# Kernel optimization log

Hardware: AMD Instinct MI355X
Metric: run time of the kernel (lower is better)

Reference implementation:

```python
import jax, jax.numpy as jnp
import numpy as np
from jax import lax


def _lstm(x, h, c, W, U, b):
    # torch LSTM gate order: i, f, g, o; b = b_ih + b_hh combined
    g = x @ W.T + h @ U.T + b
    i, f, gg, o = jnp.split(g, 4, axis=-1)
    c2 = jax.nn.sigmoid(f) * c + jax.nn.sigmoid(i) * jnp.tanh(gg)
    h2 = jax.nn.sigmoid(o) * jnp.tanh(c2)
    return h2, c2


def _run_dir(x, mask, W, U, b):
    # packed-sequence semantics: state updates only where mask, outputs 0 at pad
    B = x.shape[0]
    Hh = U.shape[1]
    h0 = jnp.zeros((B, Hh), x.dtype)

    def step(carry, inp):
        h, c = carry
        xt, mt = inp
        h2, c2 = _lstm(xt, h, c, W, U, b)
        m = mt[:, None]
        h = jnp.where(m, h2, h)
        c = jnp.where(m, c2, c)
        return (h, c), jnp.where(m, h, jnp.zeros_like(h))

    (hf, cf), outs = lax.scan(step, (h0, h0), (jnp.swapaxes(x, 0, 1), mask.T))
    return jnp.swapaxes(outs, 0, 1), hf, cf  # (B,S,H), (B,H), (B,H)


def _forward(source, source_mask, target, target_mask, emb_src, emb_tgt,
             eW0f, eU0f, eb0f, eW0b, eU0b, eb0b,
             eW1f, eU1f, eb1f, eW1b, eU1b, eb1b,
             dW0, dU0, db0, dW1, dU1, db1, wW, wb):
    x = emb_src[source]  # (B,S,D)
    finals_h, finals_c = [], []
    enc_params = [(eW0f, eU0f, eb0f, eW0b, eU0b, eb0b),
                  (eW1f, eU1f, eb1f, eW1b, eU1b, eb1b)]
    for Wf, Uf, bf, Wb, Ub, bb in enc_params:
        of, hf, cf = _run_dir(x, source_mask, Wf, Uf, bf)
        # backward direction: reverse time; prefix mask becomes suffix, so the
        # masked-update scan exactly reproduces packed reverse-direction LSTM
        ob, hb, cb = _run_dir(x[:, ::-1], source_mask[:, ::-1], Wb, Ub, bb)
        ob = ob[:, ::-1]
        x = jnp.concatenate([of, ob], axis=-1)
        finals_h.append(jnp.concatenate([hf, hb], axis=-1))  # (B, 2H)
        finals_c.append(jnp.concatenate([cf, cb], axis=-1))

    # decoder initial state: per-layer concat of fwd/bwd encoder final states
    xt = emb_tgt[target]  # (B,T,D)

    def dstep(carry, inp):
        h1, c1, h2, c2 = carry
        t, mt = inp
        m = mt[:, None]
        nh1, nc1 = _lstm(t, h1, c1, dW0, dU0, db0)
        h1 = jnp.where(m, nh1, h1)
        c1 = jnp.where(m, nc1, c1)
        nh2, nc2 = _lstm(h1, h2, c2, dW1, dU1, db1)
        h2 = jnp.where(m, nh2, h2)
        c2 = jnp.where(m, nc2, c2)
        return (h1, c1, h2, c2), jnp.where(m, h2, jnp.zeros_like(h2))

    init = (finals_h[0], finals_c[0], finals_h[1], finals_c[1])
    _, outs = lax.scan(dstep, init, (jnp.swapaxes(xt, 0, 1), target_mask.T))
    outs = jnp.swapaxes(outs, 0, 1)  # (B,T,d_out)
    return jnp.einsum('btd,vd->btv', outs, wW) + wb  # (B,T,V)


def setup_inputs() -> dict:
    key = jax.random.key(0)
    ks = jax.random.split(key, 32)
    B, S, T, V, D, H = 32, 64, 65, 32000, 256, 512
    DO = 2 * H

    def p(i, shape):
        return jax.random.normal(ks[i], shape, dtype=jnp.float32) * 0.05

    source = jax.random.randint(ks[0], (B, S), 0, V + 1)
    target = jax.random.randint(ks[1], (B, T), 0, V + 1)
    # descending-sorted lengths -> sort/perm in the original is identity
    slen = jnp.sort(jax.random.randint(ks[2], (B,), 1, S + 1))[::-1]
    tlen = jnp.sort(jax.random.randint(ks[3], (B,), 1, T + 1))[::-1]
    source_mask = jnp.arange(S)[None, :] < slen[:, None]
    target_mask = jnp.arange(T)[None, :] < tlen[:, None]
    emb = p(4, (V + 1, D))
    return dict(
        source=source, source_mask=source_mask, target=target, target_mask=target_mask,
        emb_src=emb, emb_tgt=emb + 0.0,
        eW0f=p(5, (4 * H, D)), eU0f=p(6, (4 * H, H)), eb0f=p(7, (4 * H,)),
        eW0b=p(8, (4 * H, D)), eU0b=p(9, (4 * H, H)), eb0b=p(10, (4 * H,)),
        eW1f=p(11, (4 * H, 2 * H)), eU1f=p(12, (4 * H, H)), eb1f=p(13, (4 * H,)),
        eW1b=p(14, (4 * H, 2 * H)), eU1b=p(15, (4 * H, H)), eb1b=p(16, (4 * H,)),
        dW0=p(17, (4 * DO, D)), dU0=p(18, (4 * DO, DO)), db0=p(19, (4 * DO,)),
        dW1=p(20, (4 * DO, DO)), dU1=p(21, (4 * DO, DO)), db1=p(22, (4 * DO,)),
        wW=p(23, (V, DO)), wb=p(24, (V,)))


def reference(source, source_mask, target, target_mask, emb_src, emb_tgt,
              eW0f, eU0f, eb0f, eW0b, eU0b, eb0b,
              eW1f, eU1f, eb1f, eW1b, eU1b, eb1b,
              dW0, dU0, db0, dW1, dU1, db1, wW, wb):
    return _forward(source, source_mask, target, target_mask, emb_src, emb_tgt,
                    eW0f, eU0f, eb0f, eW0b, eU0b, eb0b,
                    eW1f, eU1f, eb1f, eW1b, eU1b, eb1b,
                    dW0, dU0, db0, dW1, dU1, db1, wW, wb)
```

## Files before the change

kernel.cpp:

```cpp
#include <hip/hip_runtime.h>

#define B_ 32
#define S_ 64
#define T_ 65
#define D_ 256
#define HE 512
#define HD 1024
#define VV 32000

typedef __attribute__((ext_vector_type(8))) short bf16x8;
typedef __attribute__((ext_vector_type(4))) float f32x4;

__device__ inline unsigned short f2bf(float f) {
  unsigned int u = __float_as_uint(f);
  u += 0x7FFFu + ((u >> 16) & 1u);
  return (unsigned short)(u >> 16);
}
__device__ inline float sigmf(float x) { return 1.0f / (1.0f + __expf(-x)); }

#define MFMA16(a,b,c) __builtin_amdgcn_mfma_f32_16x16x32_bf16((a),(b),(c),0,0,0)

#define SLOT_STRIDE 32
__device__ inline void sigwait(int* slots, int* rel, int nblk, int e, int bid) {
  asm volatile("s_waitcnt vmcnt(0)" ::: "memory");
  __syncthreads();
  const int tid = threadIdx.x;
  if (bid == 0) {
    if (tid < nblk) {
      if (tid == 0)
        __hip_atomic_store(&slots[0], e, __ATOMIC_RELAXED,
                           __HIP_MEMORY_SCOPE_AGENT);
      while (__hip_atomic_load(&slots[tid * SLOT_STRIDE], __ATOMIC_RELAXED,
                               __HIP_MEMORY_SCOPE_AGENT) < e)
        __builtin_amdgcn_s_sleep(2);
    }
    __syncthreads();
    if (tid == 0)
      __hip_atomic_store(rel, e, __ATOMIC_RELAXED, __HIP_MEMORY_SCOPE_AGENT);
  } else {
    if (tid == 0) {
      __hip_atomic_store(&slots[bid * SLOT_STRIDE], e, __ATOMIC_RELAXED,
                         __HIP_MEMORY_SCOPE_AGENT);
      while (__hip_atomic_load(rel, __ATOMIC_RELAXED,
                               __HIP_MEMORY_SCOPE_AGENT) < e)
        __builtin_amdgcn_s_sleep(2);
    }
    __syncthreads();
  }
}

__device__ inline int swz(int row, int col, int LD) {
  return row * LD + ((((col >> 3) ^ (row & 7)) << 3) | (col & 7));
}
template <int LD, int NU64>
__device__ inline void stage_h(short* h_lds, const short* src) {
  unsigned long long* s = (unsigned long long*)src;
  const int tid = threadIdx.x;
#pragma unroll
  for (int base = 0; base < NU64 / 256; base += 16) {
    unsigned long long tmp[16];
#pragma unroll
    for (int i = 0; i < 16; i++) {
      if (base + i < NU64 / 256)
        tmp[i] = __hip_atomic_load(&s[(base + i) * 256 + tid], __ATOMIC_RELAXED,
                                   __HIP_MEMORY_SCOPE_AGENT);
    }
#pragma unroll
    for (int i = 0; i < 16; i++) {
      if (base + i < NU64 / 256) {
        int o = ((base + i) * 256 + tid) * 4;
        *(unsigned long long*)(h_lds + swz(o / LD, o % LD, LD)) = tmp[i];
      }
    }
  }
}

__device__ inline int mask_dtype(const unsigned char* m) {
  unsigned b0 = m[0], b1 = m[1], b2 = m[2], b3 = m[3], b4 = m[4];
  if (b0 == 1 && b1 == 1) return 0;
  if (b0 == 1) {
    if (b4 == 1) return 1;
    if (b4 == 0 && m[8] == 1) return 2;
    return 1;
  }
  if (b0 == 0x80 && b1 == 0x3F) return 4;
  if (b0 == 0x00 && b1 == 0x3C) return 5;
  if (b2 == 0x80 && b3 == 0x3F) return 3;
  return 1;
}
__device__ inline int mask_val(const unsigned char* m, int dt, int i) {
  switch (dt) {
    case 0: return m[i] != 0;
    case 1: return ((const int*)m)[i] != 0;
    case 2: return ((const long long*)m)[i] != 0;
    case 3: return ((const float*)m)[i] != 0.0f;
    default: return ((const unsigned short*)m)[i] != 0;
  }
}
__global__ void k_masks(const unsigned char* msrc, const unsigned char* mtgt,
                        signed char* o_src, signed char* o_tgt) {
  const unsigned char* m = blockIdx.x ? mtgt : msrc;
  signed char* o = blockIdx.x ? o_tgt : o_src;
  int n = blockIdx.x ? (B_ * T_) : (B_ * S_);
  int dt = mask_dtype(m);
  for (int i = threadIdx.x; i < n; i += blockDim.x)
    o[i] = (signed char)mask_val(m, dt, i);
}

struct CvtJobs {
  const float* src[13];
  short* dst[13];
  int n4[13];
};
__global__ __launch_bounds__(256) void k_convert(CvtJobs jb) {
  int j = blockIdx.y;
  const float4* s = (const float4*)jb.src[j];
  ushort4* d = (ushort4*)jb.dst[j];
  int n4 = jb.n4[j];
  for (int i = blockIdx.x * blockDim.x + threadIdx.x; i < n4;
       i += gridDim.x * blockDim.x) {
    float4 v = s[i];
    ushort4 o;
    o.x = f2bf(v.x); o.y = f2bf(v.y); o.z = f2bf(v.z); o.w = f2bf(v.w);
    d[i] = o;
  }
}

__global__ __launch_bounds__(256) void k_gather(const int* sids, const int* tids,
                                                const float* es, const float* et,
                                                short* Xs, short* Xt) {
  int job = blockIdx.y;
  int rows = job ? (B_ * T_) : (B_ * S_);
  const int* ids = job ? tids : sids;
  const float* emb = job ? et : es;
  ushort4* X = (ushort4*)(job ? Xt : Xs);
  int total = rows * (D_ / 4);
  for (int i = blockIdx.x * blockDim.x + threadIdx.x; i < total;
       i += gridDim.x * blockDim.x) {
    int row = i >> 6;
    int c4 = i & 63;
    long id = ids[row];
    float4 v = ((const float4*)(emb + id * (long)D_))[c4];
    ushort4 o;
    o.x = f2bf(v.x); o.y = f2bf(v.y); o.z = f2bf(v.z); o.w = f2bf(v.w);
    X[(long)row * 64 + c4] = o;
  }
}

template <bool B_F32, bool C_F32>
__global__ __launch_bounds__(256) void k_gemm(const short* __restrict__ A,
                                              const short* __restrict__ Bw,
                                              const float* __restrict__ Bwf,
                                              const float* __restrict__ bias,
                                              short* __restrict__ C,
                                              float* __restrict__ Cf,
                                              int M_out, int N, int K) {
  __shared__ short As[128 * 32];
  __shared__ short Bs[128 * 32];
  const int tid = threadIdx.x;
  const int wave = tid >> 6, lane = tid & 63;
  const int wm = wave >> 1, wn = wave & 1;
  const int r16 = lane & 15, kb = lane >> 4;
  const long m0 = (long)blockIdx.y * 128;
  const long n0 = (long)blockIdx.x * 128;

  const int ch0 = tid * 2, ch1 = ch0 + 1;
  const int ar0 = ch0 >> 2, ak0 = (ch0 & 3) * 8;
  const int ar1 = ch1 >> 2, ak1 = (ch1 & 3) * 8;

  f32x4 acc[4][4];
#pragma unroll
  for (int i = 0; i < 4; i++)
#pragma unroll
    for (int j = 0; j < 4; j++) acc[i][j] = (f32x4){0.f, 0.f, 0.f, 0.f};

  for (int kt = 0; kt < K; kt += 32) {
    bf16x8 va0 = *(const bf16x8*)(A + (m0 + ar0) * K + kt + ak0);
    bf16x8 va1 = *(const bf16x8*)(A + (m0 + ar1) * K + kt + ak1);
    bf16x8 vb0, vb1;
    if (B_F32) {
      const float* p0 = Bwf + (n0 + ar0) * K + kt + ak0;
      const float* p1 = Bwf + (n0 + ar1) * K + kt + ak1;
      float4 x0 = *(const float4*)p0, x1 = *(const float4*)(p0 + 4);
      float4 y0 = *(const float4*)p1, y1 = *(const float4*)(p1 + 4);
      vb0 = (bf16x8){(short)f2bf(x0.x), (short)f2bf(x0.y), (short)f2bf(x0.z),
                     (short)f2bf(x0.w), (short)f2bf(x1.x), (short)f2bf(x1.y),
                     (short)f2bf(x1.z), (short)f2bf(x1.w)};
      vb1 = (bf16x8){(short)f2bf(y0.x), (short)f2bf(y0.y), (short)f2bf(y0.z),
                     (short)f2bf(y0.w), (short)f2bf(y1.x), (short)f2bf(y1.y),
                     (short)f2bf(y1.z), (short)f2bf(y1.w)};
    } else {
      vb0 = *(const bf16x8*)(Bw + (n0 + ar0) * K + kt + ak0);
      vb1 = *(const bf16x8*)(Bw + (n0 + ar1) * K + kt + ak1);
    }
    __syncthreads();
    *(bf16x8*)(As + ar0 * 32 + ak0) = va0;
    *(bf16x8*)(As + ar1 * 32 + ak1) = va1;
    *(bf16x8*)(Bs + ar0 * 32 + ak0) = vb0;
    *(bf16x8*)(Bs + ar1 * 32 + ak1) = vb1;
    __syncthreads();
    bf16x8 av[4], bv[4];
#pragma unroll
    for (int i = 0; i < 4; i++)
      av[i] = *(const bf16x8*)(As + (wm * 64 + i * 16 + r16) * 32 + kb * 8);
#pragma unroll
    for (int j = 0; j < 4; j++)
      bv[j] = *(const bf16x8*)(Bs + (wn * 64 + j * 16 + r16) * 32 + kb * 8);
#pragma unroll
    for (int i = 0; i < 4; i++)
#pragma unroll
      for (int j = 0; j < 4; j++) acc[i][j] = MFMA16(av[i], bv[j], acc[i][j]);
  }
#pragma unroll
  for (int j = 0; j < 4; j++) {
    long gc = n0 + wn * 64 + j * 16 + r16;
    float bb = bias ? bias[gc] : 0.f;
#pragma unroll
    for (int i = 0; i < 4; i++) {
      long gr0 = m0 + wm * 64 + i * 16 + kb * 4;
#pragma unroll
      for (int r = 0; r < 4; r++) {
        long gr = gr0 + r;
        if (gr < M_out) {
          if (C_F32) Cf[gr * N + gc] = acc[i][j][r] + bb;
          else C[gr * N + gc] = (short)f2bf(acc[i][j][r] + bb);
        }
      }
    }
  }
}

__global__ __launch_bounds__(256) void k_enc_persist(
    const short* __restrict__ Wf, const short* __restrict__ Wb_,
    short* __restrict__ H, const float* __restrict__ Pf,
    const float* __restrict__ Pb, short* __restrict__ Outb, int outLD,
    int outOffDir, float* __restrict__ Cfin,
    const signed char* __restrict__ msk, int* slots, int* rel) {
  const int dir = blockIdx.y;
  const short* W = dir ? Wb_ : Wf;
  const float* P = dir ? Pb : Pf;
  int* slotsD = slots + dir * 32 * SLOT_STRIDE;
  int* relD = rel + dir * SLOT_STRIDE;
  const int q = threadIdx.x >> 6, lane = threadIdx.x & 63;
  const int r16 = lane & 15, kb = lane >> 4;
  const int n = q * HE + blockIdx.x * 16 + r16;
  const short* wr = W + (size_t)n * HE;
  const int bb = threadIdx.x >> 3;
  const int cp = threadIdx.x & 7;
  const int j0 = blockIdx.x * 16 + 2 * cp;
  __shared__ short h_lds[32 * HE];
  __shared__ float g_lds[4][2][16][16];
  float creg0 = 0.f, creg1 = 0.f;

  for (int s = 0; s < S_; ++s) {
    const int t = dir ? (S_ - 1 - s) : s;
    const int rp = s & 1;
    const short* Ar = H + ((size_t)rp * 2 + dir) * (B_ * HE);
    short* Hw = H + ((size_t)(rp ^ 1) * 2 + dir) * (B_ * HE);

    __syncthreads();
    stage_h<HE, 4096>(h_lds, Ar);
    __syncthreads();

    f32x4 acc0 = (f32x4){0.f, 0.f, 0.f, 0.f};
    f32x4 acc1 = (f32x4){0.f, 0.f, 0.f, 0.f};
#pragma unroll 8
    for (int k = kb * 8; k < HE; k += 32) {
      bf16x8 bv = *(const bf16x8*)(wr + k);
      bf16x8 a0 = *(const bf16x8*)(h_lds + swz(r16, k, HE));
      bf16x8 a1 = *(const bf16x8*)(h_lds + swz(16 + r16, k, HE));
      acc0 = MFMA16(a0, bv, acc0);
      acc1 = MFMA16(a1, bv, acc1);
    }
#pragma unroll
    for (int r = 0; r < 4; r++) {
      g_lds[q][0][kb * 4 + r][r16] = acc0[r];
      g_lds[q][1][kb * 4 + r][r16] = acc1[r];
    }
    __syncthreads();
    {
      const int mt = bb >> 4, br = bb & 15;
      const float* pr = P + (size_t)(bb * S_ + t) * (4 * HE);
      bool valid = msk[bb * S_ + t] != 0;
      unsigned int hv;
      float h2v[2];
#pragma unroll
      for (int cc = 0; cc < 2; ++cc) {
        int j = j0 + cc;
        float g0 = g_lds[0][mt][br][2 * cp + cc] + pr[j];
        float g1 = g_lds[1][mt][br][2 * cp + cc] + pr[HE + j];
        float g2 = g_lds[2][mt][br][2 * cp + cc] + pr[2 * HE + j];
        float g3 = g_lds[3][mt][br][2 * cp + cc] + pr[3 * HE + j];
        float co = cc ? creg1 : creg0;
        float c2 = sigmf(g1) * co + sigmf(g0) * tanhf(g2);
        float h2 = sigmf(g3) * tanhf(c2);
        if (valid) { if (cc) creg1 = c2; else creg0 = c2; }
        h2v[cc] = h2;
      }
      unsigned short o0 = valid ? f2bf(h2v[0])
                                : (unsigned short)h_lds[swz(bb, j0, HE)];
      unsigned short o1 = valid ? f2bf(h2v[1])
                                : (unsigned short)h_lds[swz(bb, j0 + 1, HE)];
      hv = (unsigned int)o0 | ((unsigned int)o1 << 16);
      __hip_atomic_store((unsigned int*)(Hw + bb * HE + j0), hv,
                         __ATOMIC_RELAXED, __HIP_MEMORY_SCOPE_AGENT);
      if (Outb) {
        unsigned int ov = valid ? hv : 0u;
        *(unsigned int*)(Outb + (size_t)(bb * S_ + t) * outLD +
                         outOffDir * dir + j0) = ov;
      }
    }
    if (s < S_ - 1) sigwait(slotsD, relD, 32, s + 1, blockIdx.x);
  }
  Cfin[(size_t)(dir * B_ + bb) * HE + j0] = creg0;
  Cfin[(size_t)(dir * B_ + bb) * HE + j0 + 1] = creg1;
}

__global__ __launch_bounds__(256) void k_dec_persist(
    const short* __restrict__ dU0b, const short* __restrict__ dW1b,
    const short* __restrict__ dU1b, short* __restrict__ H1,
    short* __restrict__ H2, const float* __restrict__ Q0,
    const float* __restrict__ db1f, const float* __restrict__ dC1i,
    const float* __restrict__ dC2i, short* __restrict__ douts,
    const signed char* __restrict__ msk, int* slots, int* rel) {
  const int role = blockIdx.y;
  const int bid = role * 64 + blockIdx.x;
  const int q = threadIdx.x >> 6, lane = threadIdx.x & 63;
  const int r16 = lane & 15, kb = lane >> 4;
  const int n = q * HD + blockIdx.x * 16 + r16;
  const int bb = threadIdx.x >> 3;
  const int cp = threadIdx.x & 7;
  const int j0 = blockIdx.x * 16 + 2 * cp;
  __shared__ short h_lds[32 * HD];
  __shared__ float g_lds[4][2][16][16];
  const float* Ci = role ? dC2i : dC1i;
  float creg0 = Ci[(size_t)bb * HD + j0];
  float creg1 = Ci[(size_t)bb * HD + j0 + 1];
  const short* w0 = dU0b + (size_t)n * HD;
  const short* w1 = dW1b + (size_t)n * HD;
  const short* w2 = dU1b + (size_t)n * HD;

  for (int k = 0; k <= T_; ++k) {
    if (role == 0 && k <= T_ - 1) {
      const int t = k, rp = k & 1;
      const short* Ar = H1 + (size_t)rp * (B_ * HD);
      short* Hw = H1 + (size_t)(rp ^ 1) * (B_ * HD);
      __syncthreads();
      stage_h<HD, 8192>(h_lds, Ar);
      __syncthreads();
      f32x4 acc0 = (f32x4){0.f, 0.f, 0.f, 0.f};
      f32x4 acc1 = (f32x4){0.f, 0.f, 0.f, 0.f};
#pragma unroll 8
      for (int kk = kb * 8; kk < HD; kk += 32) {
        bf16x8 bv = *(const bf16x8*)(w0 + kk);
        bf16x8 a0 = *(const bf16x8*)(h_lds + swz(r16, kk, HD));
        bf16x8 a1 = *(const bf16x8*)(h_lds + swz(16 + r16, kk, HD));
        acc0 = MFMA16(a0, bv, acc0);
        acc1 = MFMA16(a1, bv, acc1);
      }
#pragma unroll
      for (int r = 0; r < 4; r++) {
        g_lds[q][0][kb * 4 + r][r16] = acc0[r];
        g_lds[q][1][kb * 4 + r][r16] = acc1[r];
      }
      __syncthreads();
      {
        const int mt = bb >> 4, br = bb & 15;
        const float* pr = Q0 + (size_t)(bb * T_ + t) * (4 * HD);
        bool valid = msk[bb * T_ + t] != 0;
        float h2v[2];
#pragma unroll
        for (int cc = 0; cc < 2; ++cc) {
          int j = j0 + cc;
          float g0 = g_lds[0][mt][br][2 * cp + cc] + pr[j];
          float g1 = g_lds[1][mt][br][2 * cp + cc] + pr[HD + j];
          float g2 = g_lds[2][mt][br][2 * cp + cc] + pr[2 * HD + j];
          float g3 = g_lds[3][mt][br][2 * cp + cc] + pr[3 * HD + j];
          float co = cc ? creg1 : creg0;
          float c2 = sigmf(g1) * co + sigmf(g0) * tanhf(g2);
          float h2 = sigmf(g3) * tanhf(c2);
          if (valid) { if (cc) creg1 = c2; else creg0 = c2; }
          h2v[cc] = h2;
        }
        unsigned short o0 = valid ? f2bf(h2v[0])
                                  : (unsigned short)h_lds[swz(bb, j0, HD)];
        unsigned short o1 = valid ? f2bf(h2v[1])
                                  : (unsigned short)h_lds[swz(bb, j0 + 1, HD)];
        unsigned int hv = (unsigned int)o0 | ((unsigned int)o1 << 16);
        __hip_atomic_store((unsigned int*)(Hw + bb * HD + j0), hv,
                           __ATOMIC_RELAXED, __HIP_MEMORY_SCOPE_AGENT);
      }
    } else if (role == 1 && k >= 1) {
      const int t = k - 1, rp = t & 1;
      const short* X = H1 + (size_t)(k & 1) * (B_ * HD);
      const short* Ar2 = H2 + (size_t)rp * (B_ * HD);
      short* Hw = H2 + (size_t)(rp ^ 1) * (B_ * HD);
      f32x4 acc0 = (f32x4){0.f, 0.f, 0.f, 0.f};
      f32x4 acc1 = (f32x4){0.f, 0.f, 0.f, 0.f};
      __syncthreads();
      stage_h<HD, 8192>(h_lds, X);
      __syncthreads();
#pragma unroll 8
      for (int kk = kb * 8; kk < HD; kk += 32) {
        bf16x8 bv = *(const bf16x8*)(w1 + kk);
        bf16x8 a0 = *(const bf16x8*)(h_lds + swz(r16, kk, HD));
        bf16x8 a1 = *(const bf16x8*)(h_lds + swz(16 + r16, kk, HD));
        acc0 = MFMA16(a0, bv, acc0);
        acc1 = MFMA16(a1, bv, acc1);
      }
      __syncthreads();
      stage_h<HD, 8192>(h_lds, Ar2);
      __syncthreads();
#pragma unroll 8
      for (int kk = kb * 8; kk < HD; kk += 32) {
        bf16x8 bv = *(const bf16x8*)(w2 + kk);
        bf16x8 a0 = *(const bf16x8*)(h_lds + swz(r16, kk, HD));
        bf16x8 a1 = *(const bf16x8*)(h_lds + swz(16 + r16, kk, HD));
        acc0 = MFMA16(a0, bv, acc0);
        acc1 = MFMA16(a1, bv, acc1);
      }
#pragma unroll
      for (int r = 0; r < 4; r++) {
        g_lds[q][0][kb * 4 + r][r16] = acc0[r];
        g_lds[q][1][kb * 4 + r][r16] = acc1[r];
      }
      __syncthreads();
      {
        const int mt = bb >> 4, br = bb & 15;
        bool valid = msk[bb * T_ + t] != 0;
        float h2v[2];
#pragma unroll
        for (int cc = 0; cc < 2; ++cc) {
          int j = j0 + cc;
          float g0 = g_lds[0][mt][br][2 * cp + cc] + db1f[j];
          float g1 = g_lds[1][mt][br][2 * cp + cc] + db1f[HD + j];
          float g2 = g_lds[2][mt][br][2 * cp + cc] + db1f[2 * HD + j];
          float g3 = g_lds[3][mt][br][2 * cp + cc] + db1f[3 * HD + j];
          float co = cc ? creg1 : creg0;
          float c2 = sigmf(g1) * co + sigmf(g0) * tanhf(g2);
          float h2 = sigmf(g3) * tanhf(c2);
          if (valid) { if (cc) creg1 = c2; else creg0 = c2; }
          h2v[cc] = h2;
        }
        unsigned short o0 = valid ? f2bf(h2v[0])
                                  : (unsigned short)h_lds[swz(bb, j0, HD)];
        unsigned short o1 = valid ? f2bf(h2v[1])
                                  : (unsigned short)h_lds[swz(bb, j0 + 1, HD)];
        unsigned int hv = (unsigned int)o0 | ((unsigned int)o1 << 16);
        __hip_atomic_store((unsigned int*)(Hw + bb * HD + j0), hv,
                           __ATOMIC_RELAXED, __HIP_MEMORY_SCOPE_AGENT);
        *(unsigned int*)(douts + (size_t)(bb * T_ + t) * HD + j0) =
            valid ? hv : 0u;
      }
    }
    if (k < T_) sigwait(slots, rel, 128, k + 1, bid);
  }
}

__global__ __launch_bounds__(256) void k_decinit(const short* h0, const float* c0,
                                                 const short* h1, const float* c1f,
                                                 short* dh1, float* dc1,
                                                 short* dh2, float* dc2) {
  int i = blockIdx.x * 256 + threadIdx.x;
  if (i < B_ * HD) {
    int b = i >> 10, nn = i & 1023, d = nn >> 9, jj = nn & 511;
    int src = (d * B_ + b) * HE + jj;
    dh1[i] = h0[src];
    dc1[i] = c0[src];
    dh2[i] = h1[src];
    dc2[i] = c1f[src];
  }
}

extern "C" void kernel_launch(void* const* d_in, const int* in_sizes, int n_in,
                              void* d_out, int out_size, void* d_ws, size_t ws_size,
                              hipStream_t stream) {
  const int* src = (const int*)d_in[0];
  const unsigned char* msrc = (const unsigned char*)d_in[1];
  const int* tgt = (const int*)d_in[2];
  const unsigned char* mtgt = (const unsigned char*)d_in[3];
  const float* emb_s = (const float*)d_in[4];
  const float* emb_t = (const float*)d_in[5];
  const float* eW0f = (const float*)d_in[6];
  const float* eU0f = (const float*)d_in[7];
  const float* eb0f = (const float*)d_in[8];
  const float* eW0b = (const float*)d_in[9];
  const float* eU0b = (const float*)d_in[10];
  const float* eb0b = (const float*)d_in[11];
  const float* eW1f = (const float*)d_in[12];
  const float* eU1f = (const float*)d_in[13];
  const float* eb1f = (const float*)d_in[14];
  const float* eW1b = (const float*)d_in[15];
  const float* eU1b = (const float*)d_in[16];
  const float* eb1b = (const float*)d_in[17];
  const float* dW0 = (const float*)d_in[18];
  const float* dU0 = (const float*)d_in[19];
  const float* db0 = (const float*)d_in[20];
  const float* dW1 = (const float*)d_in[21];
  const float* dU1 = (const float*)d_in[22];
  const float* db1 = (const float*)d_in[23];
  const float* wW = (const float*)d_in[24];
  const float* wb = (const float*)d_in[25];
  (void)n_in; (void)in_sizes; (void)out_size; (void)ws_size;

  short* douts = (short*)d_ws;
  short* wW_b = (short*)((char*)d_ws + (size_t)2176 * 1024 * 2);

  char* po = (char*)d_out;
  size_t off = 0;
  auto alloc = [&](size_t bytes) -> char* {
    char* p = po + off;
    off += (bytes + 255) & ~(size_t)255;
    return p;
  };
  const size_t szW[12] = {
      (size_t)2048 * 256 * 2,  (size_t)2048 * 512 * 2,
      (size_t)2048 * 256 * 2,  (size_t)2048 * 512 * 2,
      (size_t)2048 * 1024 * 2, (size_t)2048 * 512 * 2,
      (size_t)2048 * 1024 * 2, (size_t)2048 * 512 * 2,
      (size_t)4096 * 256 * 2,  (size_t)4096 * 1024 * 2,
      (size_t)4096 * 1024 * 2, (size_t)4096 * 1024 * 2};
  short* Wb[12];
  for (int i = 0; i < 12; i++) Wb[i] = (short*)alloc(szW[i]);
  short* eW0f_b = Wb[0], *eU0f_b = Wb[1], *eW0b_b = Wb[2], *eU0b_b = Wb[3];
  short* eW1f_b = Wb[4], *eU1f_b = Wb[5], *eW1b_b = Wb[6], *eU1b_b = Wb[7];
  short* dW0_b = Wb[8], *dU0_b = Wb[9], *dW1_b = Wb[10], *dU1_b = Wb[11];
  short* Xs_b = (short*)alloc((size_t)2048 * 256 * 2);
  short* Xt_b = (short*)alloc((size_t)2176 * 256 * 2);
  short* X1_b = (short*)alloc((size_t)2048 * 1024 * 2);
  char* uni = alloc((size_t)2176 * 4096 * 4);
  float* P0f = (float*)uni;
  float* P0b = P0f + (size_t)2048 * 2048;
  float* P1f = (float*)uni;
  float* P1b = P1f + (size_t)2048 * 2048;
  float* Q0 = (float*)uni;
  char* zero_begin = po + off;
  int* slots_e0 = (int*)alloc(2 * 32 * SLOT_STRIDE * 4);
  int* rel_e0 = (int*)alloc(2 * SLOT_STRIDE * 4);
  int* slots_e1 = (int*)alloc(2 * 32 * SLOT_STRIDE * 4);
  int* rel_e1 = (int*)alloc(2 * SLOT_STRIDE * 4);
  int* slots_d = (int*)alloc(128 * SLOT_STRIDE * 4);
  int* rel_d = (int*)alloc(SLOT_STRIDE * 4);
  short* encH0 = (short*)alloc((size_t)2 * 2 * B_ * HE * 2);
  short* encH1 = (short*)alloc((size_t)2 * 2 * B_ * HE * 2);
  size_t zero_bytes = (size_t)((po + off) - zero_begin);
  float* Cfin0 = (float*)alloc((size_t)2 * B_ * HE * 4);
  float* Cfin1 = (float*)alloc((size_t)2 * B_ * HE * 4);
  short* dH1 = (short*)alloc((size_t)2 * B_ * HD * 2);
  short* dH2 = (short*)alloc((size_t)2 * B_ * HD * 2);
  float* dC1f = (float*)alloc((size_t)B_ * HD * 4);
  float* dC2f = (float*)alloc((size_t)B_ * HD * 4);
  signed char* msk_s = (signed char*)alloc(B_ * S_);
  signed char* msk_t = (signed char*)alloc(B_ * T_);

  const float* FN = nullptr;

  (void)hipMemsetAsync(douts, 0, (size_t)2176 * 1024 * 2, stream);
  (void)hipMemsetAsync(zero_begin, 0, zero_bytes, stream);
  k_masks<<<dim3(2), dim3(256), 0, stream>>>(msrc, mtgt, msk_s, msk_t);
  CvtJobs jb;
  const float* srcs[13] = {eW0f, eU0f, eW0b, eU0b, eW1f, eU1f,
                           eW1b, eU1b, dW0, dU0, dW1, dU1, wW};
  short* dsts[13] = {Wb[0], Wb[1], Wb[2], Wb[3], Wb[4], Wb[5],
                     Wb[6], Wb[7], Wb[8], Wb[9], Wb[10], Wb[11], wW_b};
  int ns[13] = {2048 * 256, 2048 * 512, 2048 * 256, 2048 * 512,
                2048 * 1024, 2048 * 512, 2048 * 1024, 2048 * 512,
                4096 * 256, 4096 * 1024, 4096 * 1024, 4096 * 1024, VV * 1024};
  for (int i = 0; i < 13; i++) { jb.src[i] = srcs[i]; jb.dst[i] = dsts[i]; jb.n4[i] = ns[i] / 4; }
  k_convert<<<dim3(1024, 13), 256, 0, stream>>>(jb);
  k_gather<<<dim3(544, 2), 256, 0, stream>>>(src, tgt, emb_s, emb_t, Xs_b, Xt_b);

  k_gemm<false, true><<<dim3(16, 16), 256, 0, stream>>>(
      Xs_b, eW0f_b, FN, eb0f, (short*)nullptr, P0f, 2048, 2048, 256);
  k_gemm<false, true><<<dim3(16, 16), 256, 0, stream>>>(
      Xs_b, eW0b_b, FN, eb0b, (short*)nullptr, P0b, 2048, 2048, 256);

  k_enc_persist<<<dim3(32, 2), 256, 0, stream>>>(
      eU0f_b, eU0b_b, encH0, P0f, P0b, X1_b, 1024, 512, Cfin0, msk_s,
      slots_e0, rel_e0);

  k_gemm<false, true><<<dim3(16, 16), 256, 0, stream>>>(
      X1_b, eW1f_b, FN, eb1f, (short*)nullptr, P1f, 2048, 2048, 1024);
  k_gemm<false, true><<<dim3(16, 16), 256, 0, stream>>>(
      X1_b, eW1b_b, FN, eb1b, (short*)nullptr, P1b, 2048, 2048, 1024);

  k_enc_persist<<<dim3(32, 2), 256, 0, stream>>>(
      eU1f_b, eU1b_b, encH1, P1f, P1b, (short*)nullptr, 0, 0, Cfin1, msk_s,
      slots_e1, rel_e1);

  k_decinit<<<dim3(128), 256, 0, stream>>>(encH0, Cfin0, encH1, Cfin1,
                                           dH1, dC1f, dH2, dC2f);

  k_gemm<false, true><<<dim3(32, 17), 256, 0, stream>>>(
      Xt_b, dW0_b, FN, db0, (short*)nullptr, Q0, 2176, 4096, 256);

  k_dec_persist<<<dim3(64, 2), 256, 0, stream>>>(
      dU0_b, dW1_b, dU1_b, dH1, dH2, Q0, db1, dC1f, dC2f, douts, msk_t,
      slots_d, rel_d);

  k_gemm<false, true><<<dim3(250, 17), 256, 0, stream>>>(
      douts, wW_b, FN, wb, (short*)nullptr, (float*)d_out, B_ * T_, VV, 1024);
}
```

Measured before the change: 2.175 ms.

## Use all-to-all flag barrier and stage both decoder layer-2 inputs at once

Replaces the master-block gather/release grid barrier with a flat barrier in which every block publishes its step counter and polls all peers' slots directly. This removes one serialized round trip through block 0 per recurrent step. In the decoder layer-2 role, the input h1 and recurrent h2 are staged into two separate LDS buffers in one pass, and a single interleaved MFMA loop replaces the two sequential staging and compute phases. This removes a barrier and staging round, but doubles decoder LDS use to about 128KB per block and adds polling traffic from every block.

```diff
diff --git a/kernel.cpp b/kernel.cpp
--- a/kernel.cpp
+++ b/kernel.cpp
@@ -21,56 +21,68 @@
 #define MFMA16(a,b,c) __builtin_amdgcn_mfma_f32_16x16x32_bf16((a),(b),(c),0,0,0)
 
 #define SLOT_STRIDE 32
-__device__ inline void sigwait(int* slots, int* rel, int nblk, int e, int bid) {
+__device__ inline void gbar_all(int* slots, int nblk, int e, int bid) {
   asm volatile("s_waitcnt vmcnt(0)" ::: "memory");
   __syncthreads();
   const int tid = threadIdx.x;
-  if (bid == 0) {
-    if (tid < nblk) {
-      if (tid == 0)
-        __hip_atomic_store(&slots[0], e, __ATOMIC_RELAXED,
-                           __HIP_MEMORY_SCOPE_AGENT);
-      while (__hip_atomic_load(&slots[tid * SLOT_STRIDE], __ATOMIC_RELAXED,
-                               __HIP_MEMORY_SCOPE_AGENT) < e)
-        __builtin_amdgcn_s_sleep(2);
-    }
-    __syncthreads();
-    if (tid == 0)
-      __hip_atomic_store(rel, e, __ATOMIC_RELAXED, __HIP_MEMORY_SCOPE_AGENT);
-  } else {
-    if (tid == 0) {
-      __hip_atomic_store(&slots[bid * SLOT_STRIDE], e, __ATOMIC_RELAXED,
-                         __HIP_MEMORY_SCOPE_AGENT);
-      while (__hip_atomic_load(rel, __ATOMIC_RELAXED,
-                               __HIP_MEMORY_SCOPE_AGENT) < e)
-        __builtin_amdgcn_s_sleep(2);
-    }
-    __syncthreads();
-  }
+  if (tid == 0)
+    __hip_atomic_store(&slots[bid * SLOT_STRIDE], e, __ATOMIC_RELAXED,
+                       __HIP_MEMORY_SCOPE_AGENT);
+  if (tid < nblk) {
+    while (__hip_atomic_load(&slots[tid * SLOT_STRIDE], __ATOMIC_RELAXED,
+                             __HIP_MEMORY_SCOPE_AGENT) < e)
+      __builtin_amdgcn_s_sleep(2);
+  }
+  __syncthreads();
 }
 
 __device__ inline int swz(int row, int col, int LD) {
   return row * LD + ((((col >> 3) ^ (row & 7)) << 3) | (col & 7));
 }
 template <int LD, int NU64>
-__device__ inline void stage_h(short* h_lds, const short* src) {
-  unsigned long long* s = (unsigned long long*)src;
+__device__ inline void stage1(short* lds, const short* src) {
+  const unsigned long long* s = (const unsigned long long*)src;
   const int tid = threadIdx.x;
-#pragma unroll
-  for (int base = 0; base < NU64 / 256; base += 16) {
-    unsigned long long tmp[16];
-#pragma unroll
-    for (int i = 0; i < 16; i++) {
-      if (base + i < NU64 / 256)
-        tmp[i] = __hip_atomic_load(&s[(base + i) * 256 + tid], __ATOMIC_RELAXED,
-                                   __HIP_MEMORY_SCOPE_AGENT);
-    }
-#pragma unroll
-    for (int i = 0; i < 16; i++) {
-      if (base + i < NU64 / 256) {
-        int o = ((base + i) * 256 + tid) * 4;
-        *(unsigned long long*)(h_lds + swz(o / LD, o % LD, LD)) = tmp[i];
-      }
+  constexpr int NPT = NU64 / 256;
+  unsigned long long tmp[NPT];
+#pragma unroll
+  for (int i = 0; i < NPT; i++)
+    tmp[i] = __hip_atomic_load(&s[i * 256 + tid], __ATOMIC_RELAXED,
+                               __HIP_MEMORY_SCOPE_AGENT);
+#pragma unroll
+  for (int i = 0; i < NPT; i++) {
+    int o = (i * 256 + tid) * 4;
+    *(unsigned long long*)(lds + swz(o / LD, o % LD, LD)) = tmp[i];
+  }
+}
+template <int LD, int NU64>
+__device__ inline void stage2(short* lds1, const short* src1, short* lds2,
+                              const short* src2) {
+  const unsigned long long* s1 = (const unsigned long long*)src1;
+  const unsigned long long* s2 = (const unsigned long long*)src2;
+  const int tid = threadIdx.x;
+  constexpr int NPT = NU64 / 256;
+  constexpr int HALF = NPT / 2;
+#pragma unroll
+  for (int h = 0; h < 2; h++) {
+    unsigned long long t1[HALF], t2[HALF];
+#pragma unroll
+    for (int i = 0; i < HALF; i++)
+      t1[i] = __hip_atomic_load(&s1[(h * HALF + i) * 256 + tid],
+                                __ATOMIC_RELAXED, __HIP_MEMORY_SCOPE_AGENT);
+#pragma unroll
+    for (int i = 0; i < HALF; i++)
+      t2[i] = __hip_atomic_load(&s2[(h * HALF + i) * 256 + tid],
+                                __ATOMIC_RELAXED, __HIP_MEMORY_SCOPE_AGENT);
+#pragma unroll
+    for (int i = 0; i < HALF; i++) {
+      int o = ((h * HALF + i) * 256 + tid) * 4;
+      *(unsigned long long*)(lds1 + swz(o / LD, o % LD, LD)) = t1[i];
+    }
+#pragma unroll
+    for (int i = 0; i < HALF; i++) {
+      int o = ((h * HALF + i) * 256 + tid) * 4;
+      *(unsigned long long*)(lds2 + swz(o / LD, o % LD, LD)) = t2[i];
     }
   }
 }
@@ -235,12 +247,11 @@
     short* __restrict__ H, const float* __restrict__ Pf,
     const float* __restrict__ Pb, short* __restrict__ Outb, int outLD,
     int outOffDir, float* __restrict__ Cfin,
-    const signed char* __restrict__ msk, int* slots, int* rel) {
+    const signed char* __restrict__ msk, int* slots) {
   const int dir = blockIdx.y;
   const short* W = dir ? Wb_ : Wf;
   const float* P = dir ? Pb : Pf;
   int* slotsD = slots + dir * 32 * SLOT_STRIDE;
-  int* relD = rel + dir * SLOT_STRIDE;
   const int q = threadIdx.x >> 6, lane = threadIdx.x & 63;
   const int r16 = lane & 15, kb = lane >> 4;
   const int n = q * HE + blockIdx.x * 16 + r16;
@@ -259,7 +270,7 @@
     short* Hw = H + ((size_t)(rp ^ 1) * 2 + dir) * (B_ * HE);
 
     __syncthreads();
-    stage_h<HE, 4096>(h_lds, Ar);
+    stage1<HE, 4096>(h_lds, Ar);
     __syncthreads();
 
     f32x4 acc0 = (f32x4){0.f, 0.f, 0.f, 0.f};
@@ -310,7 +321,7 @@
                          outOffDir * dir + j0) = ov;
       }
     }
-    if (s < S_ - 1) sigwait(slotsD, relD, 32, s + 1, blockIdx.x);
+    if (s < S_ - 1) gbar_all(slotsD, 32, s + 1, blockIdx.x);
   }
   Cfin[(size_t)(dir * B_ + bb) * HE + j0] = creg0;
   Cfin[(size_t)(dir * B_ + bb) * HE + j0 + 1] = creg1;
@@ -322,7 +333,7 @@
     short* __restrict__ H2, const float* __restrict__ Q0,
     const float* __restrict__ db1f, const float* __restrict__ dC1i,
     const float* __restrict__ dC2i, short* __restrict__ douts,
-    const signed char* __restrict__ msk, int* slots, int* rel) {
+    const signed char* __restrict__ msk, int* slots) {
   const int role = blockIdx.y;
   const int bid = role * 64 + blockIdx.x;
   const int q = threadIdx.x >> 6, lane = threadIdx.x & 63;
@@ -331,7 +342,8 @@
   const int bb = threadIdx.x >> 3;
   const int cp = threadIdx.x & 7;
   const int j0 = blockIdx.x * 16 + 2 * cp;
-  __shared__ short h_lds[32 * HD];
+  __shared__ short h_lds1[32 * HD];
+  __shared__ short h_lds2[32 * HD];
   __shared__ float g_lds[4][2][16][16];
   const float* Ci = role ? dC2i : dC1i;
   float creg0 = Ci[(size_t)bb * HD + j0];
@@ -346,15 +358,15 @@
       const short* Ar = H1 + (size_t)rp * (B_ * HD);
       short* Hw = H1 + (size_t)(rp ^ 1) * (B_ * HD);
       __syncthreads();
-      stage_h<HD, 8192>(h_lds, Ar);
+      stage1<HD, 8192>(h_lds1, Ar);
       __syncthreads();
       f32x4 acc0 = (f32x4){0.f, 0.f, 0.f, 0.f};
       f32x4 acc1 = (f32x4){0.f, 0.f, 0.f, 0.f};
 #pragma unroll 8
       for (int kk = kb * 8; kk < HD; kk += 32) {
         bf16x8 bv = *(const bf16x8*)(w0 + kk);
-        bf16x8 a0 = *(const bf16x8*)(h_lds + swz(r16, kk, HD));
-        bf16x8 a1 = *(const bf16x8*)(h_lds + swz(16 + r16, kk, HD));
+        bf16x8 a0 = *(const bf16x8*)(h_lds1 + swz(r16, kk, HD));
+        bf16x8 a1 = *(const bf16x8*)(h_lds1 + swz(16 + r16, kk, HD));
         acc0 = MFMA16(a0, bv, acc0);
         acc1 = MFMA16(a1, bv, acc1);
       }
@@ -383,9 +395,9 @@
           h2v[cc] = h2;
         }
         unsigned short o0 = valid ? f2bf(h2v[0])
-                                  : (unsigned short)h_lds[swz(bb, j0, HD)];
+                                  : (unsigned short)h_lds1[swz(bb, j0, HD)];
         unsigned short o1 = valid ? f2bf(h2v[1])
-                                  : (unsigned short)h_lds[swz(bb, j0 + 1, HD)];
+                                  : (unsigned short)h_lds1[swz(bb, j0 + 1, HD)];
         unsigned int hv = (unsigned int)o0 | ((unsigned int)o1 << 16);
         __hip_atomic_store((unsigned int*)(Hw + bb * HD + j0), hv,
                            __ATOMIC_RELAXED, __HIP_MEMORY_SCOPE_AGENT);
@@ -395,29 +407,23 @@
       const short* X = H1 + (size_t)(k & 1) * (B_ * HD);
       const short* Ar2 = H2 + (size_t)rp * (B_ * HD);
       short* Hw = H2 + (size_t)(rp ^ 1) * (B_ * HD);
+      __syncthreads();
+      stage2<HD, 8192>(h_lds1, X, h_lds2, Ar2);
+      __syncthreads();
       f32x4 acc0 = (f32x4){0.f, 0.f, 0.f, 0.f};
       f32x4 acc1 = (f32x4){0.f, 0.f, 0.f, 0.f};
-      __syncthreads();
-      stage_h<HD, 8192>(h_lds, X);
-      __syncthreads();
-#pragma unroll 8
+#pragma unroll 4
       for (int kk = kb * 8; kk < HD; kk += 32) {
-        bf16x8 bv = *(const bf16x8*)(w1 + kk);
-        bf16x8 a0 = *(const bf16x8*)(h_lds + swz(r16, kk, HD));
-        bf16x8 a1 = *(const bf16x8*)(h_lds + swz(16 + r16, kk, HD));
-        acc0 = MFMA16(a0, bv, acc0);
-        acc1 = MFMA16(a1, bv, acc1);
-      }
-      __syncthreads();
-      stage_h<HD, 8192>(h_lds, Ar2);
-      __syncthreads();
-#pragma unroll 8
-      for (int kk = kb * 8; kk < HD; kk += 32) {
-        bf16x8 bv = *(const bf16x8*)(w2 + kk);
-        bf16x8 a0 = *(const bf16x8*)(h_lds + swz(r16, kk, HD));
-        bf16x8 a1 = *(const bf16x8*)(h_lds + swz(16 + r16, kk, HD));
-        acc0 = MFMA16(a0, bv, acc0);
-        acc1 = MFMA16(a1, bv, acc1);
+        bf16x8 bv1 = *(const bf16x8*)(w1 + kk);
+        bf16x8 a0 = *(const bf16x8*)(h_lds1 + swz(r16, kk, HD));
+        bf16x8 a1 = *(const bf16x8*)(h_lds1 + swz(16 + r16, kk, HD));
+        acc0 = MFMA16(a0, bv1, acc0);
+        acc1 = MFMA16(a1, bv1, acc1);
+        bf16x8 bv2 = *(const bf16x8*)(w2 + kk);
+        bf16x8 b0 = *(const bf16x8*)(h_lds2 + swz(r16, kk, HD));
+        bf16x8 b1 = *(const bf16x8*)(h_lds2 + swz(16 + r16, kk, HD));
+        acc0 = MFMA16(b0, bv2, acc0);
+        acc1 = MFMA16(b1, bv2, acc1);
       }
 #pragma unroll
       for (int r = 0; r < 4; r++) {
@@ -443,9 +449,9 @@
           h2v[cc] = h2;
         }
         unsigned short o0 = valid ? f2bf(h2v[0])
-                                  : (unsigned short)h_lds[swz(bb, j0, HD)];
+                                  : (unsigned short)h_lds2[swz(bb, j0, HD)];
         unsigned short o1 = valid ? f2bf(h2v[1])
-                                  : (unsigned short)h_lds[swz(bb, j0 + 1, HD)];
+                                  : (unsigned short)h_lds2[swz(bb, j0 + 1, HD)];
         unsigned int hv = (unsigned int)o0 | ((unsigned int)o1 << 16);
         __hip_atomic_store((unsigned int*)(Hw + bb * HD + j0), hv,
                            __ATOMIC_RELAXED, __HIP_MEMORY_SCOPE_AGENT);
@@ -453,7 +459,7 @@
             valid ? hv : 0u;
       }
     }
-    if (k < T_) sigwait(slots, rel, 128, k + 1, bid);
+    if (k < T_) gbar_all(slots, 128, k + 1, bid);
   }
 }
 
@@ -536,11 +542,8 @@
   float* Q0 = (float*)uni;
   char* zero_begin = po + off;
   int* slots_e0 = (int*)alloc(2 * 32 * SLOT_STRIDE * 4);
-  int* rel_e0 = (int*)alloc(2 * SLOT_STRIDE * 4);
   int* slots_e1 = (int*)alloc(2 * 32 * SLOT_STRIDE * 4);
-  int* rel_e1 = (int*)alloc(2 * SLOT_STRIDE * 4);
   int* slots_d = (int*)alloc(128 * SLOT_STRIDE * 4);
-  int* rel_d = (int*)alloc(SLOT_STRIDE * 4);
   short* encH0 = (short*)alloc((size_t)2 * 2 * B_ * HE * 2);
   short* encH1 = (short*)alloc((size_t)2 * 2 * B_ * HE * 2);
   size_t zero_bytes = (size_t)((po + off) - zero_begin);
@@ -576,8 +579,7 @@
       Xs_b, eW0b_b, FN, eb0b, (short*)nullptr, P0b, 2048, 2048, 256);
 
   k_enc_persist<<<dim3(32, 2), 256, 0, stream>>>(
-      eU0f_b, eU0b_b, encH0, P0f, P0b, X1_b, 1024, 512, Cfin0, msk_s,
-      slots_e0, rel_e0);
+      eU0f_b, eU0b_b, encH0, P0f, P0b, X1_b, 1024, 512, Cfin0, msk_s, slots_e0);
 
   k_gemm<false, true><<<dim3(16, 16), 256, 0, stream>>>(
       X1_b, eW1f_b, FN, eb1f, (short*)nullptr, P1f, 2048, 2048, 1024);
@@ -586,7 +588,7 @@
 
   k_enc_persist<<<dim3(32, 2), 256, 0, stream>>>(
       eU1f_b, eU1b_b, encH1, P1f, P1b, (short*)nullptr, 0, 0, Cfin1, msk_s,
-      slots_e1, rel_e1);
+      slots_e1);
 
   k_decinit<<<dim3(128), 256, 0, stream>>>(encH0, Cfin0, encH1, Cfin1,
                                            dH1, dC1f, dH2, dC2f);
@@ -596,7 +598,7 @@
 
   k_dec_persist<<<dim3(64, 2), 256, 0, stream>>>(
       dU0_b, dW1_b, dU1_b, dH1, dH2, Q0, db1, dC1f, dC2f, douts, msk_t,
-      slots_d, rel_d);
+      slots_d);
 
   k_gemm<false, true><<<dim3(250, 17), 256, 0, stream>>>(
       douts, wW_b, FN, wb, (short*)nullptr, (float*)d_out, B_ * T_, VV, 1024);
```

Measured after the change: 1.979 ms. 9.0% less time.
